# Kernel optimization log

Hardware: AMD Instinct MI355X
Metric: run time of the kernel (lower is better)

Reference implementation:

```python
import jax, jax.numpy as jnp
import numpy as np

EPS = 1e-08
ORDINAL = 2.0

def setup_inputs() -> dict:
    key = jax.random.key(0)
    k1, k2, k3, k4, k5 = jax.random.split(key, 5)
    B, IN, OUT = 1024, 256, 1024
    inputs = jax.random.normal(k1, (B, IN), dtype=jnp.float32)
    weights = jax.random.normal(k2, (OUT, IN), dtype=jnp.float32) * (1.0 / np.sqrt(IN))
    biases = jax.random.normal(k3, (OUT,), dtype=jnp.float32) * (1.0 / np.sqrt(IN))
    centers = jax.random.normal(k4, (OUT, IN), dtype=jnp.float32) * 0.1
    # diag inv covars ~ U(3/(IN+0.5), 3/(IN-0.5)) per reset_parameters
    inv_covars = jax.random.uniform(k5, (OUT, IN), dtype=jnp.float32,
                                    minval=3.0 / (IN + 0.5), maxval=3.0 / (IN - 0.5))
    return {"inputs": inputs, "weights": weights, "biases": biases,
            "centers": centers, "inv_covars": inv_covars}

def reference(inputs, weights, biases, centers, inv_covars):
    # linear part: [B, OUT]
    l = inputs @ weights.T + biases
    # diag covar path (ordinal = 2.0, so the 1e-32 stabilizer is absent and
    # pow(c^2, 1/ordinal) == |c| after clamping):
    # g[b, z] = sum_i ( |x[b,i] - c[z,i]| * sqrt(clamp(ic[z,i])^2) )^2
    ic = jnp.minimum(inv_covars, 1.0 / EPS)
    scale = jnp.power(ic * ic, 1.0 / ORDINAL)  # [OUT, IN]
    diff = jnp.abs(inputs[:, None, :] - centers[None, :, :]) * scale[None, :, :]  # [B, OUT, IN]
    g = jnp.exp(-jnp.sum(jnp.power(diff, ORDINAL), axis=-1))  # [B, OUT]
    res = l * g
    return (res, g)
```

## Files before the change

### kernel.cpp

```cpp
#include <hip/hip_runtime.h>
#include <math.h>


typedef __attribute__((ext_vector_type(8))) short short8;
typedef __attribute__((ext_vector_type(4))) float floatx4;

#define BDIM   1024
#define INDIM  256
#define OUTDIM 1024
#define AK     512
#define WK     256
#define GK     512

__device__ __forceinline__ unsigned short f2bf(float f) {
    union { float f; unsigned u; } v; v.f = f;
    unsigned r = v.u + 0x7FFFu + ((v.u >> 16) & 1u);
    return (unsigned short)(r >> 16);
}

__global__ __launch_bounds__(256)
void fgn_prep(const float* __restrict__ X, const float* __restrict__ W,
              const float* __restrict__ C, const float* __restrict__ IC,
              unsigned short* __restrict__ Ap, unsigned short* __restrict__ Wb,
              unsigned short* __restrict__ Gw, float* __restrict__ Cz)
{
    const int bid = blockIdx.x;
    if (bid < 256) {
        const int f   = bid * 256 + threadIdx.x;
        const int row = f >> 6;
        const int kq  = (f & 63) << 2;
        float4 x = *(const float4*)&X[row * INDIM + kq];
        ushort4 a, b;
        a.x = f2bf(x.x);      a.y = f2bf(x.y);      a.z = f2bf(x.z);      a.w = f2bf(x.w);
        b.x = f2bf(x.x*x.x);  b.y = f2bf(x.y*x.y);  b.z = f2bf(x.z*x.z);  b.w = f2bf(x.w*x.w);
        *(ushort4*)&Ap[row * AK + kq]         = a;
        *(ushort4*)&Ap[row * AK + INDIM + kq] = b;
    } else {
        const int z    = (bid - 256) * 4 + (threadIdx.x >> 6);
        const int lane = threadIdx.x & 63;
        const int k    = lane << 2;
        float4 w  = *(const float4*)&W [z * INDIM + k];
        float4 c  = *(const float4*)&C [z * INDIM + k];
        float4 ic = *(const float4*)&IC[z * INDIM + k];
        float s0 = fminf(ic.x, 1e8f), s1 = fminf(ic.y, 1e8f);
        float s2 = fminf(ic.z, 1e8f), s3 = fminf(ic.w, 1e8f);
        float q0 = s0*s0, q1 = s1*s1, q2 = s2*s2, q3 = s3*s3;
        ushort4 wv, w2v, s2v;
        wv.x  = f2bf(w.x);            wv.y  = f2bf(w.y);
        wv.z  = f2bf(w.z);            wv.w  = f2bf(w.w);
        w2v.x = f2bf(-2.f*c.x*q0);    w2v.y = f2bf(-2.f*c.y*q1);
        w2v.z = f2bf(-2.f*c.z*q2);    w2v.w = f2bf(-2.f*c.w*q3);
        s2v.x = f2bf(q0);             s2v.y = f2bf(q1);
        s2v.z = f2bf(q2);             s2v.w = f2bf(q3);
        *(ushort4*)&Wb[z * WK + k]         = wv;
        *(ushort4*)&Gw[z * GK + k]         = w2v;
        *(ushort4*)&Gw[z * GK + INDIM + k] = s2v;
        float cc = c.x*c.x*q0 + c.y*c.y*q1 + c.z*c.z*q2 + c.w*c.w*q3;
        #pragma unroll
        for (int off = 32; off; off >>= 1) cc += __shfl_xor(cc, off);
        if (lane == 0) Cz[z] = cc;
    }
}

__global__ __launch_bounds__(64)
void fgn_main(const unsigned short* __restrict__ Ap, const unsigned short* __restrict__ Wb,
              const unsigned short* __restrict__ Gw, const float* __restrict__ Bias,
              const float* __restrict__ Cz, float* __restrict__ Out)
{
    const int n0   = blockIdx.x * 32;
    const int m0   = blockIdx.y * 32;
    const int lane = threadIdx.x;
    const int r    = lane & 15;
    const int q    = lane >> 4;

    const short8* A0 = (const short8*)(Ap + (size_t)(m0 +      r) * AK) + q;
    const short8* A1 = (const short8*)(Ap + (size_t)(m0 + 16 + r) * AK) + q;
    const short8* G0 = (const short8*)(Gw + (size_t)(n0 +      r) * GK) + q;
    const short8* G1 = (const short8*)(Gw + (size_t)(n0 + 16 + r) * GK) + q;
    const short8* W0 = (const short8*)(Wb + (size_t)(n0 +      r) * WK) + q;
    const short8* W1 = (const short8*)(Wb + (size_t)(n0 + 16 + r) * WK) + q;

    floatx4 zero = {0.f, 0.f, 0.f, 0.f};
    floatx4 accL[2][2] = {{zero, zero}, {zero, zero}};
    floatx4 accG[2][2] = {{zero, zero}, {zero, zero}};

    #pragma unroll
    for (int kk = 0; kk < 8; ++kk) {
        short8 a0 = A0[kk * 4];
        short8 a1 = A1[kk * 4];
        short8 g0 = G0[kk * 4];
        short8 g1 = G1[kk * 4];
        short8 w0 = W0[kk * 4];
        short8 w1 = W1[kk * 4];
        accG[0][0] = __builtin_amdgcn_mfma_f32_16x16x32_bf16(a0, g0, accG[0][0], 0, 0, 0);
        accG[0][1] = __builtin_amdgcn_mfma_f32_16x16x32_bf16(a0, g1, accG[0][1], 0, 0, 0);
        accG[1][0] = __builtin_amdgcn_mfma_f32_16x16x32_bf16(a1, g0, accG[1][0], 0, 0, 0);
        accG[1][1] = __builtin_amdgcn_mfma_f32_16x16x32_bf16(a1, g1, accG[1][1], 0, 0, 0);
        accL[0][0] = __builtin_amdgcn_mfma_f32_16x16x32_bf16(a0, w0, accL[0][0], 0, 0, 0);
        accL[0][1] = __builtin_amdgcn_mfma_f32_16x16x32_bf16(a0, w1, accL[0][1], 0, 0, 0);
        accL[1][0] = __builtin_amdgcn_mfma_f32_16x16x32_bf16(a1, w0, accL[1][0], 0, 0, 0);
        accL[1][1] = __builtin_amdgcn_mfma_f32_16x16x32_bf16(a1, w1, accL[1][1], 0, 0, 0);
    }
    #pragma unroll
    for (int kk = 8; kk < 16; ++kk) {
        short8 a0 = A0[kk * 4];
        short8 a1 = A1[kk * 4];
        short8 g0 = G0[kk * 4];
        short8 g1 = G1[kk * 4];
        accG[0][0] = __builtin_amdgcn_mfma_f32_16x16x32_bf16(a0, g0, accG[0][0], 0, 0, 0);
        accG[0][1] = __builtin_amdgcn_mfma_f32_16x16x32_bf16(a0, g1, accG[0][1], 0, 0, 0);
        accG[1][0] = __builtin_amdgcn_mfma_f32_16x16x32_bf16(a1, g0, accG[1][0], 0, 0, 0);
        accG[1][1] = __builtin_amdgcn_mfma_f32_16x16x32_bf16(a1, g1, accG[1][1], 0, 0, 0);
    }

    float bias[2], cz[2];
    bias[0] = Bias[n0 + r];      bias[1] = Bias[n0 + 16 + r];
    cz[0]   = Cz[n0 + r];        cz[1]   = Cz[n0 + 16 + r];
    float* OutR = Out;
    float* OutG = Out + (size_t)BDIM * OUTDIM;
    #pragma unroll
    for (int mt = 0; mt < 2; ++mt) {
        #pragma unroll
        for (int nt = 0; nt < 2; ++nt) {
            const int n = n0 + nt * 16 + r;
            #pragma unroll
            for (int reg = 0; reg < 4; ++reg) {
                const int m = m0 + mt * 16 + q * 4 + reg;
                float gexp = expf(-(accG[mt][nt][reg] + cz[nt]));
                float l    = accL[mt][nt][reg] + bias[nt];
                OutR[(size_t)m * OUTDIM + n] = l * gexp;
                OutG[(size_t)m * OUTDIM + n] = gexp;
            }
        }
    }
}

extern "C" void kernel_launch(void* const* d_in, const int* in_sizes, int n_in,
                              void* d_out, int out_size, void* d_ws, size_t ws_size,
                              hipStream_t stream) {
    const float* X    = (const float*)d_in[0];
    const float* W    = (const float*)d_in[1];
    const float* Bias = (const float*)d_in[2];
    const float* C    = (const float*)d_in[3];
    const float* IC   = (const float*)d_in[4];
    float* Out = (float*)d_out;

    unsigned short* Ap = (unsigned short*)d_ws;
    unsigned short* Wb = Ap + (size_t)BDIM * AK;
    unsigned short* Gw = Wb + (size_t)OUTDIM * WK;
    float*          Cz = (float*)(Gw + (size_t)OUTDIM * GK);

    fgn_prep<<<512, 256, 0, stream>>>(X, W, C, IC, Ap, Wb, Gw, Cz);
    dim3 grid(OUTDIM / 32, BDIM / 32);
    fgn_main<<<grid, 64, 0, stream>>>(Ap, Wb, Gw, Bias, Cz, Out);
}
```

Baseline: 76.83 us.

## Split K across four waves per block with LDS reduction

Each 32x32 output tile is now computed by four wavefronts instead of one. Each wave handles a quarter of the K dimension for the Gaussian GEMM, and two of the waves also cover the linear GEMM. Partial accumulators are reduced through padded shared memory before the exp and the stores. This shortens the serial MFMA chain per wave and adds latency hiding, at the cost of LDS traffic, a barrier, and divergent work across the waves.

```diff
diff --git a/kernel.cpp b/kernel.cpp
--- a/kernel.cpp
+++ b/kernel.cpp
@@ -62,47 +62,36 @@
     }
 }
 
-__global__ __launch_bounds__(64)
+__global__ __launch_bounds__(256)
 void fgn_main(const unsigned short* __restrict__ Ap, const unsigned short* __restrict__ Wb,
               const unsigned short* __restrict__ Gw, const float* __restrict__ Bias,
               const float* __restrict__ Cz, float* __restrict__ Out)
 {
     const int n0   = blockIdx.x * 32;
     const int m0   = blockIdx.y * 32;
-    const int lane = threadIdx.x;
+    const int t    = threadIdx.x;
+    const int w    = t >> 6;
+    const int lane = t & 63;
     const int r    = lane & 15;
     const int q    = lane >> 4;
 
-    const short8* A0 = (const short8*)(Ap + (size_t)(m0 +      r) * AK) + q;
-    const short8* A1 = (const short8*)(Ap + (size_t)(m0 + 16 + r) * AK) + q;
-    const short8* G0 = (const short8*)(Gw + (size_t)(n0 +      r) * GK) + q;
-    const short8* G1 = (const short8*)(Gw + (size_t)(n0 + 16 + r) * GK) + q;
-    const short8* W0 = (const short8*)(Wb + (size_t)(n0 +      r) * WK) + q;
-    const short8* W1 = (const short8*)(Wb + (size_t)(n0 + 16 + r) * WK) + q;
+    __shared__ float sL[2 * 64 * 17];
+    __shared__ float sG[4 * 64 * 17];
+
+    const int kb = w * 16;
+    const short8* A0 = (const short8*)(Ap + (size_t)(m0 +      r) * AK) + q + kb;
+    const short8* A1 = (const short8*)(Ap + (size_t)(m0 + 16 + r) * AK) + q + kb;
+    const short8* G0 = (const short8*)(Gw + (size_t)(n0 +      r) * GK) + q + kb;
+    const short8* G1 = (const short8*)(Gw + (size_t)(n0 + 16 + r) * GK) + q + kb;
+    const short8* W0 = (const short8*)(Wb + (size_t)(n0 +      r) * WK) + q + kb;
+    const short8* W1 = (const short8*)(Wb + (size_t)(n0 + 16 + r) * WK) + q + kb;
 
     floatx4 zero = {0.f, 0.f, 0.f, 0.f};
     floatx4 accL[2][2] = {{zero, zero}, {zero, zero}};
     floatx4 accG[2][2] = {{zero, zero}, {zero, zero}};
 
     #pragma unroll
-    for (int kk = 0; kk < 8; ++kk) {
-        short8 a0 = A0[kk * 4];
-        short8 a1 = A1[kk * 4];
-        short8 g0 = G0[kk * 4];
-        short8 g1 = G1[kk * 4];
-        short8 w0 = W0[kk * 4];
-        short8 w1 = W1[kk * 4];
-        accG[0][0] = __builtin_amdgcn_mfma_f32_16x16x32_bf16(a0, g0, accG[0][0], 0, 0, 0);
-        accG[0][1] = __builtin_amdgcn_mfma_f32_16x16x32_bf16(a0, g1, accG[0][1], 0, 0, 0);
-        accG[1][0] = __builtin_amdgcn_mfma_f32_16x16x32_bf16(a1, g0, accG[1][0], 0, 0, 0);
-        accG[1][1] = __builtin_amdgcn_mfma_f32_16x16x32_bf16(a1, g1, accG[1][1], 0, 0, 0);
-        accL[0][0] = __builtin_amdgcn_mfma_f32_16x16x32_bf16(a0, w0, accL[0][0], 0, 0, 0);
-        accL[0][1] = __builtin_amdgcn_mfma_f32_16x16x32_bf16(a0, w1, accL[0][1], 0, 0, 0);
-        accL[1][0] = __builtin_amdgcn_mfma_f32_16x16x32_bf16(a1, w0, accL[1][0], 0, 0, 0);
-        accL[1][1] = __builtin_amdgcn_mfma_f32_16x16x32_bf16(a1, w1, accL[1][1], 0, 0, 0);
-    }
-    #pragma unroll
-    for (int kk = 8; kk < 16; ++kk) {
+    for (int kk = 0; kk < 4; ++kk) {
         short8 a0 = A0[kk * 4];
         short8 a1 = A1[kk * 4];
         short8 g0 = G0[kk * 4];
@@ -111,27 +100,48 @@
         accG[0][1] = __builtin_amdgcn_mfma_f32_16x16x32_bf16(a0, g1, accG[0][1], 0, 0, 0);
         accG[1][0] = __builtin_amdgcn_mfma_f32_16x16x32_bf16(a1, g0, accG[1][0], 0, 0, 0);
         accG[1][1] = __builtin_amdgcn_mfma_f32_16x16x32_bf16(a1, g1, accG[1][1], 0, 0, 0);
+        if (w < 2) {
+            short8 w0 = W0[kk * 4];
+            short8 w1 = W1[kk * 4];
+            accL[0][0] = __builtin_amdgcn_mfma_f32_16x16x32_bf16(a0, w0, accL[0][0], 0, 0, 0);
+            accL[0][1] = __builtin_amdgcn_mfma_f32_16x16x32_bf16(a0, w1, accL[0][1], 0, 0, 0);
+            accL[1][0] = __builtin_amdgcn_mfma_f32_16x16x32_bf16(a1, w0, accL[1][0], 0, 0, 0);
+            accL[1][1] = __builtin_amdgcn_mfma_f32_16x16x32_bf16(a1, w1, accL[1][1], 0, 0, 0);
+        }
     }
 
-    float bias[2], cz[2];
-    bias[0] = Bias[n0 + r];      bias[1] = Bias[n0 + 16 + r];
-    cz[0]   = Cz[n0 + r];        cz[1]   = Cz[n0 + 16 + r];
+    #pragma unroll
+    for (int mt = 0; mt < 2; ++mt)
+        #pragma unroll
+        for (int nt = 0; nt < 2; ++nt)
+            #pragma unroll
+            for (int reg = 0; reg < 4; ++reg) {
+                const int f = mt * 8 + nt * 4 + reg;
+                sG[(w * 64 + lane) * 17 + f] = accG[mt][nt][reg];
+                if (w < 2) sL[(w * 64 + lane) * 17 + f] = accL[mt][nt][reg];
+            }
+    __syncthreads();
+
+    const int l  = lane;
+    const int gr = w;
+    const int li = l & 15;
+    const float bias0 = Bias[n0 + li],  bias1 = Bias[n0 + 16 + li];
+    const float cz0   = Cz[n0 + li],    cz1   = Cz[n0 + 16 + li];
     float* OutR = Out;
     float* OutG = Out + (size_t)BDIM * OUTDIM;
     #pragma unroll
-    for (int mt = 0; mt < 2; ++mt) {
-        #pragma unroll
-        for (int nt = 0; nt < 2; ++nt) {
-            const int n = n0 + nt * 16 + r;
-            #pragma unroll
-            for (int reg = 0; reg < 4; ++reg) {
-                const int m = m0 + mt * 16 + q * 4 + reg;
-                float gexp = expf(-(accG[mt][nt][reg] + cz[nt]));
-                float l    = accL[mt][nt][reg] + bias[nt];
-                OutR[(size_t)m * OUTDIM + n] = l * gexp;
-                OutG[(size_t)m * OUTDIM + n] = gexp;
-            }
-        }
+    for (int j = 0; j < 4; ++j) {
+        const int f = gr * 4 + j;
+        const float Ls = sL[l * 17 + f] + sL[(64 + l) * 17 + f];
+        const float Gs = sG[l * 17 + f]         + sG[(64 + l) * 17 + f]
+                       + sG[(128 + l) * 17 + f] + sG[(192 + l) * 17 + f];
+        const int mt = f >> 3, nt = (f >> 2) & 1, reg = f & 3;
+        const int m = m0 + mt * 16 + (l >> 4) * 4 + reg;
+        const int n = n0 + nt * 16 + li;
+        const float g   = expf(-(Gs + (nt ? cz1 : cz0)));
+        const float res = (Ls + (nt ? bias1 : bias0)) * g;
+        OutR[(size_t)m * OUTDIM + n] = res;
+        OutG[(size_t)m * OUTDIM + n] = g;
     }
 }
 
@@ -152,5 +162,5 @@
 
     fgn_prep<<<512, 256, 0, stream>>>(X, W, C, IC, Ap, Wb, Gw, Cz);
     dim3 grid(OUTDIM / 32, BDIM / 32);
-    fgn_main<<<grid, 64, 0, stream>>>(Ap, Wb, Gw, Bias, Cz, Out);
+    fgn_main<<<grid, 256, 0, stream>>>(Ap, Wb, Gw, Bias, Cz, Out);
 }
```

Measured after the change: 77.49 us. About the same (+0.9%).
